# Kernel tuning notes

Measured on AMD Instinct MI355X. Metric: run time of the kernel, lower is better.

The kernel has to match this reference:

```python
import jax, jax.numpy as jnp
import numpy as np


def setup_inputs() -> dict:
    key = jax.random.key(0)
    ks = jax.random.split(key, 4)
    B, S, H = 1, 2048, 2048
    E, I = 32, 768
    scale_h = 1.0 / np.sqrt(H)
    scale_i = 1.0 / np.sqrt(I)
    return {
        "hidden_states": jax.random.normal(ks[0], (B, S, H), dtype=jnp.float32),
        "gate_w": jax.random.normal(ks[1], (E, H), dtype=jnp.float32) * scale_h,
        "gate_up_proj": jax.random.normal(ks[2], (E, H, 2 * I), dtype=jnp.float32) * scale_h,
        "down_proj": jax.random.normal(ks[3], (E, I, H), dtype=jnp.float32) * scale_i,
    }


TOP_K = 4


def reference(hidden_states, gate_w, gate_up_proj, down_proj):
    B, S, H = hidden_states.shape
    x = hidden_states.reshape(-1, H)                      # [T, H]
    T = x.shape[0]

    # Router: softmax -> top-k -> renormalize -> scatter back to dense [T, E]
    router_logits = x @ gate_w.T                          # [T, E]
    probs = jax.nn.softmax(router_logits.astype(jnp.float32), axis=-1)
    top_w, top_idx = jax.lax.top_k(probs, TOP_K)          # [T, K]
    top_w = top_w / jnp.sum(top_w, axis=-1, keepdims=True)
    top_w = top_w.astype(x.dtype)
    router_weights = jnp.zeros_like(router_logits).at[
        jnp.arange(T)[:, None], top_idx
    ].set(top_w)                                          # [T, E]

    # Experts (eval path): every expert processes every token, then weight & sum.
    gate_up = jnp.einsum("th,ehi->eti", x, gate_up_proj)  # [E, T, 2I]
    gate, up = jnp.split(gate_up, 2, axis=-1)
    h = up * jax.nn.silu(gate)                            # [E, T, I]
    expert_out = jnp.einsum("eti,eih->eth", h, down_proj)  # [E, T, H]
    out = jnp.einsum("eth,te->th", expert_out, router_weights)  # [T, H]

    return out.reshape(B, S, H), router_logits
```

## Files before the change

### kernel.cpp

```cpp
#include <hip/hip_runtime.h>
#include <hip/hip_bf16.h>

#define T_TOK 2048
#define H_DIM 2048
#define E_NUM 32
#define I_DIM 768
#define TOPK  4
#define S4    (T_TOK * TOPK)

typedef __attribute__((ext_vector_type(8))) short bf16x8;
typedef __attribute__((ext_vector_type(4))) float f32x4;

__device__ __forceinline__ unsigned pk2(float a, float b) {
    __hip_bfloat16 ha = __float2bfloat16(a);
    __hip_bfloat16 hb = __float2bfloat16(b);
    unsigned short ua = *(unsigned short*)&ha;
    unsigned short ub = *(unsigned short*)&hb;
    return (unsigned)ua | ((unsigned)ub << 16);
}

#define MFMA16(a, b, c) __builtin_amdgcn_mfma_f32_16x16x32_bf16(a, b, c, 0, 0, 0)

__global__ __launch_bounds__(64) void router_kernel(
    const float* __restrict__ x, const float* __restrict__ gate_w,
    float* __restrict__ logits_out, int* __restrict__ cnt,
    int* __restrict__ tok_list, float* __restrict__ tok_w,
    int* __restrict__ tok_slots)
{
    const int t = blockIdx.x;
    const int lane = threadIdx.x;
    __shared__ float xs[H_DIM];
    const float4* __restrict__ xv = (const float4*)(x + (size_t)t * H_DIM);
    float4* xsv = (float4*)xs;
#pragma unroll
    for (int i = 0; i < H_DIM / 4 / 64; ++i) xsv[lane + i * 64] = xv[lane + i * 64];
    __syncthreads();

    const int e = lane & 31;
    const int half = lane >> 5;
    const float4* __restrict__ wv = (const float4*)(gate_w + (size_t)e * H_DIM) + half * (H_DIM / 8);
    const float4* __restrict__ xh = ((const float4*)xs) + half * (H_DIM / 8);
    float acc = 0.f;
#pragma unroll 4
    for (int i = 0; i < H_DIM / 8; ++i) {
        float4 w4 = wv[i], x4 = xh[i];
        acc += w4.x * x4.x + w4.y * x4.y + w4.z * x4.z + w4.w * x4.w;
    }
    acc += __shfl_xor(acc, 32, 64);
    if (lane < 32) logits_out[(size_t)t * E_NUM + e] = acc;

    float v = acc;
    float topv[TOPK]; int topi[TOPK];
#pragma unroll
    for (int r = 0; r < TOPK; ++r) {
        float bv = v; int bi = e;
#pragma unroll
        for (int off = 16; off >= 1; off >>= 1) {
            float ov = __shfl_xor(bv, off, 32);
            int   oi = __shfl_xor(bi, off, 32);
            if (ov > bv || (ov == bv && oi < bi)) { bv = ov; bi = oi; }
        }
        topv[r] = bv; topi[r] = bi;
        if (e == bi) v = -1e30f;
    }
    if (lane == 0) {
        float w[TOPK]; float s = 0.f;
#pragma unroll
        for (int r = 0; r < TOPK; ++r) { w[r] = expf(topv[r] - topv[0]); s += w[r]; }
        float inv = 1.f / s;
#pragma unroll
        for (int r = 0; r < TOPK; ++r) {
            int pos = atomicAdd(&cnt[topi[r]], 1);
            tok_list[topi[r] * T_TOK + pos] = t;
            tok_w  [topi[r] * T_TOK + pos] = w[r] * inv;
            tok_slots[t * TOPK + r] = (topi[r] << 12) | pos;
        }
    }
}

__global__ void scan_kernel(const int* __restrict__ cnt, int* __restrict__ slot_base)
{
    if (threadIdx.x == 0) {
        int s = 0;
        for (int e = 0; e < E_NUM; ++e) { slot_base[e] = s; s += cnt[e]; }
        slot_base[E_NUM] = s;
    }
}

__global__ __launch_bounds__(256) void gather_kernel(
    const float* __restrict__ x, const int* __restrict__ cnt,
    const int* __restrict__ slot_base, const int* __restrict__ tok_list,
    unsigned short* __restrict__ xg_t)
{
    const int e = blockIdx.x;
    const int count = cnt[e];
    const int m0 = blockIdx.y * 8;
    if (m0 >= count) return;
    const int s8   = threadIdx.x >> 5;
    const int kc31 = threadIdx.x & 31;
    const int m = m0 + s8;
    if (m >= count) return;
    const int tok  = tok_list[e * T_TOK + m];
    const int slot = slot_base[e] + m;
    const float* __restrict__ src = x + (size_t)tok * H_DIM;
#pragma unroll
    for (int kcq = 0; kcq < 8; ++kcq) {
        const int kc = kcq * 32 + kc31;
        float4 a = *(const float4*)(src + kc * 8);
        float4 b = *(const float4*)(src + kc * 8 + 4);
        uint4 o;
        o.x = pk2(a.x, a.y); o.y = pk2(a.z, a.w);
        o.z = pk2(b.x, b.y); o.w = pk2(b.z, b.w);
        *(uint4*)(xg_t + ((size_t)kc * S4 + slot) * 8) = o;
    }
}

#define GU_NC (H_DIM / 64)
__global__ __launch_bounds__(512, 2) void gateup_mfma(
    const unsigned short* __restrict__ xg_t, const float* __restrict__ gup_w,
    const int* __restrict__ cnt, const int* __restrict__ slot_base,
    const float* __restrict__ tok_w, unsigned short* __restrict__ h_t)
{
    const int e  = blockIdx.x;
    const int nt = blockIdx.y;
    const int mt = blockIdx.z;
    const int count = cnt[e];
    if (mt * 256 >= count) return;
    const int tid  = threadIdx.x;
    const int lane = tid & 63;
    const int w    = tid >> 6;
    const int base = slot_base[e];
    const int l16  = lane & 15, lg = lane >> 4;

    __shared__ unsigned short Bls[2][2][4 * 192 * 8];
    __shared__ float wls[256];

    if (tid < 256) {
        int m = mt * 256 + tid; if (m >= count) m = count - 1;
        wls[tid] = tok_w[e * T_TOK + m];
    }

    int m0 = mt * 256 + w * 32 + l16;      if (m0 >= count) m0 = count - 1;
    int m1 = mt * 256 + w * 32 + 16 + l16; if (m1 >= count) m1 = count - 1;
    const unsigned short* a0b = xg_t + (size_t)(base + m0) * 8;
    const unsigned short* a1b = xg_t + (size_t)(base + m1) * 8;

    const int bhalf = tid >> 8;
    const int t8    = tid & 255;
    const int kb    = (t8 >> 3) * 2;
    const int n4    = (t8 & 7) * 4;
    const int sq    = kb >> 5;
    const int lgb   = (kb >> 3) & 3;
    const int k8    = kb & 7;
    const float* __restrict__ bbase =
        gup_w + ((size_t)e * H_DIM + kb) * (2 * I_DIM) + (size_t)bhalf * I_DIM + nt * 96 + n4;

    float4 sv0[3], sv1[3];
    bf16x8 aR[4];

#define GU_ALOAD(C) do { _Pragma("unroll") for (int s = 0; s < 2; ++s) { \
        const size_t ao_ = (size_t)((C) * 8 + s * 4 + lg) * (S4 * 8); \
        aR[s]     = *(const bf16x8*)(a0b + ao_); \
        aR[2 + s] = *(const bf16x8*)(a1b + ao_); } } while (0)
#define GU_LOAD(C) do { _Pragma("unroll") for (int j = 0; j < 3; ++j) { \
        const float* s_ = bbase + (size_t)(C) * 64 * (2 * I_DIM) + j * 32; \
        sv0[j] = *(const float4*)s_; \
        sv1[j] = *(const float4*)(s_ + 2 * I_DIM); } } while (0)
#define GU_WRITE(BUF) do { _Pragma("unroll") for (int j = 0; j < 3; ++j) { \
        unsigned short* bw_ = &Bls[BUF][sq][(lgb * 192 + bhalf * 96 + j * 32 + n4) * 8 + k8]; \
        float p0[4] = {sv0[j].x, sv0[j].y, sv0[j].z, sv0[j].w}; \
        float p1[4] = {sv1[j].x, sv1[j].y, sv1[j].z, sv1[j].w}; \
        _Pragma("unroll") for (int q = 0; q < 4; ++q) \
            *(unsigned*)&bw_[q * 8] = pk2(p0[q], p1[q]); } } while (0)

    f32x4 accg[2][6], accu[2][6];
#pragma unroll
    for (int i = 0; i < 2; ++i)
#pragma unroll
        for (int f = 0; f < 6; ++f) { accg[i][f] = {0.f,0.f,0.f,0.f}; accu[i][f] = {0.f,0.f,0.f,0.f}; }

    GU_LOAD(0);
    GU_WRITE(0);

    for (int c = 0; c < GU_NC; ++c) {
        const int buf = c & 1;
        const bool pf = (c + 1 < GU_NC);
        __syncthreads();
        GU_ALOAD(c);
        if (pf) GU_LOAD(c + 1);
#pragma unroll
        for (int s = 0; s < 2; ++s) {
            bf16x8 a0 = aR[s];
            bf16x8 a1 = aR[2 + s];
            const unsigned short* bs_ = &Bls[buf][s][(lg * 192) * 8];
#pragma unroll
            for (int f = 0; f < 6; ++f) {
                bf16x8 bg = *(const bf16x8*)(bs_ + (f * 16 + l16) * 8);
                bf16x8 bu = *(const bf16x8*)(bs_ + (96 + f * 16 + l16) * 8);
                accg[0][f] = MFMA16(a0, bg, accg[0][f]);
                accg[1][f] = MFMA16(a1, bg, accg[1][f]);
                accu[0][f] = MFMA16(a0, bu, accu[0][f]);
                accu[1][f] = MFMA16(a1, bu, accu[1][f]);
            }
        }
        if (pf) GU_WRITE(buf ^ 1);
    }
#undef GU_ALOAD
#undef GU_LOAD
#undef GU_WRITE

#pragma unroll
    for (int i = 0; i < 2; ++i) {
        const int mloc = w * 32 + i * 16 + lg * 4;
#pragma unroll
        for (int r = 0; r < 4; ++r) {
            const int mrow = mt * 256 + mloc + r;
            if (mrow < count) {
                const float wgt = wls[mloc + r];
                const size_t slot = (size_t)(base + mrow);
#pragma unroll
                for (int f = 0; f < 6; ++f) {
                    const int col = nt * 96 + f * 16 + l16;
                    float g = accg[i][f][r], u = accu[i][f][r];
                    float sv = g / (1.f + expf(-g));
                    __hip_bfloat16 hb = __float2bfloat16(wgt * u * sv);
                    h_t[((size_t)(col >> 3) * S4 + slot) * 8 + (col & 7)] = *(unsigned short*)&hb;
                }
            }
        }
    }
}

#define DN_NC (I_DIM / 32)
__global__ __launch_bounds__(512, 2) void down_mfma(
    const unsigned short* __restrict__ h_t, const float* __restrict__ down_w,
    const int* __restrict__ cnt, const int* __restrict__ slot_base,
    float* __restrict__ ods)
{
    const int e  = blockIdx.x;
    const int nt = blockIdx.y;
    const int mt = blockIdx.z;
    const int count = cnt[e];
    if (mt * 256 >= count) return;
    const int tid  = threadIdx.x;
    const int lane = tid & 63;
    const int w    = tid >> 6;
    const int base = slot_base[e];
    const int l16  = lane & 15, lg = lane >> 4;

    __shared__ unsigned short Bls[2][4 * 256 * 8];

    int m0 = mt * 256 + w * 32 + l16;      if (m0 >= count) m0 = count - 1;
    int m1 = mt * 256 + w * 32 + 16 + l16; if (m1 >= count) m1 = count - 1;
    const unsigned short* a0b = h_t + (size_t)(base + m0) * 8;
    const unsigned short* a1b = h_t + (size_t)(base + m1) * 8;

    const int kb  = (tid >> 5) * 2;
    const int n4  = (tid & 31) * 4;
    const int lgb = kb >> 3;
    const int k8  = kb & 7;
    const float* __restrict__ bbase =
        down_w + ((size_t)e * I_DIM + kb) * H_DIM + nt * 256 + n4;

    float4 sv0[2], sv1[2];
    bf16x8 aR[2];

#define DN_ALOAD(C) do { \
        const size_t ao_ = (size_t)((C) * 4 + lg) * (S4 * 8); \
        aR[0] = *(const bf16x8*)(a0b + ao_); \
        aR[1] = *(const bf16x8*)(a1b + ao_); } while (0)
#define DN_LOAD(C) do { _Pragma("unroll") for (int j = 0; j < 2; ++j) { \
        const float* s_ = bbase + (size_t)(C) * 32 * H_DIM + j * 128; \
        sv0[j] = *(const float4*)s_; \
        sv1[j] = *(const float4*)(s_ + H_DIM); } } while (0)
#define DN_WRITE(BUF) do { _Pragma("unroll") for (int j = 0; j < 2; ++j) { \
        unsigned short* bw_ = &Bls[BUF][(lgb * 256 + j * 128 + n4) * 8 + k8]; \
        float p0[4] = {sv0[j].x, sv0[j].y, sv0[j].z, sv0[j].w}; \
        float p1[4] = {sv1[j].x, sv1[j].y, sv1[j].z, sv1[j].w}; \
        _Pragma("unroll") for (int q = 0; q < 4; ++q) \
            *(unsigned*)&bw_[q * 8] = pk2(p0[q], p1[q]); } } while (0)

    f32x4 acc[2][16];
#pragma unroll
    for (int i = 0; i < 2; ++i)
#pragma unroll
        for (int f = 0; f < 16; ++f) acc[i][f] = {0.f,0.f,0.f,0.f};

    DN_LOAD(0);
    DN_WRITE(0);

    for (int c = 0; c < DN_NC; ++c) {
        const int buf = c & 1;
        const bool pf = (c + 1 < DN_NC);
        __syncthreads();
        DN_ALOAD(c);
        if (pf) DN_LOAD(c + 1);
        {
            bf16x8 a0 = aR[0];
            bf16x8 a1 = aR[1];
            const unsigned short* bs_ = &Bls[buf][(lg * 256) * 8];
#pragma unroll
            for (int f = 0; f < 16; ++f) {
                bf16x8 b = *(const bf16x8*)(bs_ + (f * 16 + l16) * 8);
                acc[0][f] = MFMA16(a0, b, acc[0][f]);
                acc[1][f] = MFMA16(a1, b, acc[1][f]);
            }
        }
        if (pf) DN_WRITE(buf ^ 1);
    }
#undef DN_ALOAD
#undef DN_LOAD
#undef DN_WRITE

#pragma unroll
    for (int i = 0; i < 2; ++i) {
        const int mloc = w * 32 + i * 16 + lg * 4;
#pragma unroll
        for (int r = 0; r < 4; ++r) {
            const int mrow = mt * 256 + mloc + r;
            if (mrow < count) {
                float* orow = ods + (size_t)(base + mrow) * H_DIM + nt * 256;
#pragma unroll
                for (int f = 0; f < 16; ++f)
                    orow[f * 16 + l16] = acc[i][f][r];
            }
        }
    }
}

__global__ __launch_bounds__(256) void combine_kernel(
    const float* __restrict__ ods, const int* __restrict__ tok_slots,
    const int* __restrict__ slot_base, float* __restrict__ out)
{
    const int t = blockIdx.x;
    const int c0 = threadIdx.x * 8;
    const float* rows[TOPK];
#pragma unroll
    for (int r = 0; r < TOPK; ++r) {
        const int pk = tok_slots[t * TOPK + r];
        const int e = pk >> 12, pos = pk & 4095;
        rows[r] = ods + (size_t)(slot_base[e] + pos) * H_DIM + c0;
    }
    float4 a0 = {0.f,0.f,0.f,0.f}, a1 = {0.f,0.f,0.f,0.f};
#pragma unroll
    for (int r = 0; r < TOPK; ++r) {
        float4 v0 = *(const float4*)(rows[r]);
        float4 v1 = *(const float4*)(rows[r] + 4);
        a0.x += v0.x; a0.y += v0.y; a0.z += v0.z; a0.w += v0.w;
        a1.x += v1.x; a1.y += v1.y; a1.z += v1.z; a1.w += v1.w;
    }
    float* o = out + (size_t)t * H_DIM + c0;
    *(float4*)o = a0;
    *(float4*)(o + 4) = a1;
}

extern "C" void kernel_launch(void* const* d_in, const int* in_sizes, int n_in,
                              void* d_out, int out_size, void* d_ws, size_t ws_size,
                              hipStream_t stream) {
    const float* x      = (const float*)d_in[0];
    const float* gate_w = (const float*)d_in[1];
    const float* gup_w  = (const float*)d_in[2];
    const float* down_w = (const float*)d_in[3];
    float* out    = (float*)d_out;

    char* wsp = (char*)d_ws;
    int*   cnt       = (int*)(wsp);
    int*   slot_base = (int*)(wsp + 256);
    int*   tok_list  = (int*)(wsp + 4096);
    float* tok_w     = (float*)(wsp + 4096 + (size_t)E_NUM * T_TOK * 4);
    int*   tok_slots = (int*)(wsp + (768u << 10));

    size_t off = (size_t)1 << 20;
    unsigned short* xg_t = (unsigned short*)(wsp + off); off += (size_t)S4 * H_DIM * 2;
    unsigned short* h_t  = (unsigned short*)(wsp + off); off += (size_t)S4 * I_DIM * 2;
    float*          ods  = (float*)(wsp + off);          off += (size_t)S4 * H_DIM * 4;

    hipMemsetAsync(cnt, 0, 256, stream);

    router_kernel<<<T_TOK, 64, 0, stream>>>(x, gate_w, out + (size_t)T_TOK * H_DIM,
                                            cnt, tok_list, tok_w, tok_slots);
    scan_kernel<<<1, 64, 0, stream>>>(cnt, slot_base);
    gather_kernel<<<dim3(E_NUM, 256), 256, 0, stream>>>(x, cnt, slot_base, tok_list, xg_t);
    gateup_mfma<<<dim3(E_NUM, 8, 8), 512, 0, stream>>>(
        xg_t, gup_w, cnt, slot_base, tok_w, h_t);
    down_mfma<<<dim3(E_NUM, 8, 8), 512, 0, stream>>>(
        h_t, down_w, cnt, slot_base, ods);
    combine_kernel<<<T_TOK, 256, 0, stream>>>(ods, tok_slots, slot_base, out);
}
```

Baseline: 434.8 us.

## Store down-projection outputs in bf16 and pad gate-up LDS rows

The per-slot down-projection results are now written as bf16 instead of fp32, and the combine kernel reads them as bf16 and widens them to float. This halves the traffic of the large intermediate buffer, at the cost of rounding each expert contribution before summation. Separately, the gate-up LDS tile rows are padded by one 8-element group to reduce bank conflicts on the MFMA B-operand reads.

```diff
diff --git a/kernel.cpp b/kernel.cpp
--- a/kernel.cpp
+++ b/kernel.cpp
@@ -17,6 +17,11 @@
     unsigned short ua = *(unsigned short*)&ha;
     unsigned short ub = *(unsigned short*)&hb;
     return (unsigned)ua | ((unsigned)ub << 16);
+}
+
+__device__ __forceinline__ float bf2f(unsigned short u) {
+    unsigned v = (unsigned)u << 16;
+    return *(float*)&v;
 }
 
 #define MFMA16(a, b, c) __builtin_amdgcn_mfma_f32_16x16x32_bf16(a, b, c, 0, 0, 0)
@@ -116,6 +121,7 @@
 }
 
 #define GU_NC (H_DIM / 64)
+#define GU_RS (193 * 8)
 __global__ __launch_bounds__(512, 2) void gateup_mfma(
     const unsigned short* __restrict__ xg_t, const float* __restrict__ gup_w,
     const int* __restrict__ cnt, const int* __restrict__ slot_base,
@@ -132,7 +138,7 @@
     const int base = slot_base[e];
     const int l16  = lane & 15, lg = lane >> 4;
 
-    __shared__ unsigned short Bls[2][2][4 * 192 * 8];
+    __shared__ unsigned short Bls[2][2][4 * GU_RS];
     __shared__ float wls[256];
 
     if (tid < 256) {
@@ -167,7 +173,7 @@
         sv0[j] = *(const float4*)s_; \
         sv1[j] = *(const float4*)(s_ + 2 * I_DIM); } } while (0)
 #define GU_WRITE(BUF) do { _Pragma("unroll") for (int j = 0; j < 3; ++j) { \
-        unsigned short* bw_ = &Bls[BUF][sq][(lgb * 192 + bhalf * 96 + j * 32 + n4) * 8 + k8]; \
+        unsigned short* bw_ = &Bls[BUF][sq][lgb * GU_RS + (bhalf * 96 + j * 32 + n4) * 8 + k8]; \
         float p0[4] = {sv0[j].x, sv0[j].y, sv0[j].z, sv0[j].w}; \
         float p1[4] = {sv1[j].x, sv1[j].y, sv1[j].z, sv1[j].w}; \
         _Pragma("unroll") for (int q = 0; q < 4; ++q) \
@@ -192,7 +198,7 @@
         for (int s = 0; s < 2; ++s) {
             bf16x8 a0 = aR[s];
             bf16x8 a1 = aR[2 + s];
-            const unsigned short* bs_ = &Bls[buf][s][(lg * 192) * 8];
+            const unsigned short* bs_ = &Bls[buf][s][lg * GU_RS];
 #pragma unroll
             for (int f = 0; f < 6; ++f) {
                 bf16x8 bg = *(const bf16x8*)(bs_ + (f * 16 + l16) * 8);
@@ -235,7 +241,7 @@
 __global__ __launch_bounds__(512, 2) void down_mfma(
     const unsigned short* __restrict__ h_t, const float* __restrict__ down_w,
     const int* __restrict__ cnt, const int* __restrict__ slot_base,
-    float* __restrict__ ods)
+    unsigned short* __restrict__ ods)
 {
     const int e  = blockIdx.x;
     const int nt = blockIdx.y;
@@ -319,39 +325,43 @@
         for (int r = 0; r < 4; ++r) {
             const int mrow = mt * 256 + mloc + r;
             if (mrow < count) {
-                float* orow = ods + (size_t)(base + mrow) * H_DIM + nt * 256;
-#pragma unroll
-                for (int f = 0; f < 16; ++f)
-                    orow[f * 16 + l16] = acc[i][f][r];
+                unsigned short* orow = ods + (size_t)(base + mrow) * H_DIM + nt * 256;
+#pragma unroll
+                for (int f = 0; f < 16; ++f) {
+                    __hip_bfloat16 hb = __float2bfloat16(acc[i][f][r]);
+                    orow[f * 16 + l16] = *(unsigned short*)&hb;
+                }
             }
         }
     }
 }
 
 __global__ __launch_bounds__(256) void combine_kernel(
-    const float* __restrict__ ods, const int* __restrict__ tok_slots,
+    const unsigned short* __restrict__ ods, const int* __restrict__ tok_slots,
     const int* __restrict__ slot_base, float* __restrict__ out)
 {
     const int t = blockIdx.x;
     const int c0 = threadIdx.x * 8;
-    const float* rows[TOPK];
+    const unsigned short* rows[TOPK];
 #pragma unroll
     for (int r = 0; r < TOPK; ++r) {
         const int pk = tok_slots[t * TOPK + r];
         const int e = pk >> 12, pos = pk & 4095;
         rows[r] = ods + (size_t)(slot_base[e] + pos) * H_DIM + c0;
     }
-    float4 a0 = {0.f,0.f,0.f,0.f}, a1 = {0.f,0.f,0.f,0.f};
+    float s[8] = {0.f, 0.f, 0.f, 0.f, 0.f, 0.f, 0.f, 0.f};
 #pragma unroll
     for (int r = 0; r < TOPK; ++r) {
-        float4 v0 = *(const float4*)(rows[r]);
-        float4 v1 = *(const float4*)(rows[r] + 4);
-        a0.x += v0.x; a0.y += v0.y; a0.z += v0.z; a0.w += v0.w;
-        a1.x += v1.x; a1.y += v1.y; a1.z += v1.z; a1.w += v1.w;
+        uint4 v = *(const uint4*)(rows[r]);
+        const unsigned short* u = (const unsigned short*)&v;
+#pragma unroll
+        for (int k = 0; k < 8; ++k) s[k] += bf2f(u[k]);
     }
     float* o = out + (size_t)t * H_DIM + c0;
-    *(float4*)o = a0;
-    *(float4*)(o + 4) = a1;
+    float4 o0 = {s[0], s[1], s[2], s[3]};
+    float4 o1 = {s[4], s[5], s[6], s[7]};
+    *(float4*)o = o0;
+    *(float4*)(o + 4) = o1;
 }
 
 extern "C" void kernel_launch(void* const* d_in, const int* in_sizes, int n_in,
@@ -373,7 +383,7 @@
     size_t off = (size_t)1 << 20;
     unsigned short* xg_t = (unsigned short*)(wsp + off); off += (size_t)S4 * H_DIM * 2;
     unsigned short* h_t  = (unsigned short*)(wsp + off); off += (size_t)S4 * I_DIM * 2;
-    float*          ods  = (float*)(wsp + off);          off += (size_t)S4 * H_DIM * 4;
+    unsigned short* ods  = (unsigned short*)(wsp + off); off += (size_t)S4 * H_DIM * 2;
 
     hipMemsetAsync(cnt, 0, 256, stream);
 
```

After: 422.5 us, median of 2. 2.8% less time.
